# Performance work log

Measured on AMD Instinct MI355X. Metric: run time of the kernel, lower is better.

## Reference

```python
import jax, jax.numpy as jnp
import numpy as np

B, S, K_IN = 8, 2048, 512
D_MODEL, N_INPUT, N_PROCESS = 1024, 4096, 2048
K = 256


def setup_inputs() -> dict:
    key = jax.random.key(0)
    k1, k2, k3, k4 = jax.random.split(key, 4)
    return {
        "selected_activations": jax.random.normal(k1, (B, S, K_IN), dtype=jnp.float32),
        "selected_indices": jax.random.randint(k2, (B, K_IN), 0, N_INPUT, dtype=jnp.int64),
        "k": K,
        "combination_weights": jax.random.normal(k3, (N_PROCESS, N_INPUT), dtype=jnp.float32),
        "output_projections": jax.random.normal(k4, (N_PROCESS, D_MODEL), dtype=jnp.float32),
    }


def reference(selected_activations, selected_indices, k, combination_weights, output_projections):
    # Gather per-batch combination weights: [n_process, B, k_in] -> [B, n_process, k_in]
    sel_w = jnp.take(combination_weights, selected_indices, axis=1)  # [P, B, k_in]
    sel_w = jnp.transpose(sel_w, (1, 0, 2))                          # [B, P, k_in]
    # Batched matmul + exact GELU (torch F.gelu default is erf-based)
    process_act = jax.nn.gelu(
        jnp.einsum("bsk,bpk->bsp", selected_activations, sel_w), approximate=False
    )  # [B, S, P]
    # Top-k gating over mean activation across sequence
    process_scores = process_act.mean(axis=1)                        # [B, P]
    _, proc_idx = jax.lax.top_k(process_scores, k)                   # [B, k]
    # Gather selected process activations along last dim
    sel_proc_act = jnp.take_along_axis(process_act, proc_idx[:, None, :], axis=2)  # [B, S, k]
    # Gather output projections per batch: [B, k, d_model]
    sel_proj = output_projections[proc_idx]                          # [B, k, D]
    return jnp.einsum("bsk,bkd->bsd", sel_proc_act, sel_proj)        # [B, S, D]
```

## Files before the change

### kernel.cpp

```cpp
#include <hip/hip_runtime.h>
#include <hip/hip_bf16.h>
#include <math.h>

#define B_    8
#define S_    2048
#define KIN_  512
#define NIN_  4096
#define P_    2048
#define D_    1024
#define KSEL_ 256

typedef __attribute__((ext_vector_type(8))) short short8;
typedef __attribute__((ext_vector_type(4))) float f32x4;

__device__ __forceinline__ unsigned short f2bf(float f) {
    unsigned u = __float_as_uint(f);
    unsigned r = (u + 0x7fffu + ((u >> 16) & 1u)) >> 16;
    return (unsigned short)r;
}
__device__ __forceinline__ float bf2f(unsigned short h) {
    return __uint_as_float(((unsigned)h) << 16);
}
__device__ __forceinline__ float gelu_exact(float x) {
    return 0.5f * x * (1.0f + erff(x * 0.70710678118654752f));
}
__device__ __forceinline__ void gl2lds16(const void* g, void* l) {
    __builtin_amdgcn_global_load_lds(
        (const __attribute__((address_space(1))) unsigned int*)g,
        (__attribute__((address_space(3))) unsigned int*)l, 16, 0, 0);
}


__global__ __launch_bounds__(256) void prep_kernel(
        const float* __restrict__ A, const float* __restrict__ W,
        const int* __restrict__ idx,
        unsigned short* __restrict__ Ahi, unsigned short* __restrict__ AloF,
        unsigned short* __restrict__ Ghi, unsigned short* __restrict__ Glo) {
    __shared__ int ibs[KIN_];
    int id = blockIdx.x;
    int t  = threadIdx.x;
    if (id < 1024) {
        int b = id >> 7, rb = id & 127;
        int l = t & 63, wv = t >> 6;
        int lr = l & 15, quad = l >> 4;
        const float* src = A + ((size_t)(b * S_ + rb * 16 + lr)) * KIN_ + quad * 8;
        unsigned short* dh = Ahi + ((size_t)(b * S_ + rb * 16 + lr)) * KIN_ + quad * 8;
        unsigned short* dl = AloF + (size_t)b * 1048576 + (size_t)rb * 512 + (size_t)l * 8;
        for (int kb = wv; kb < 16; kb += 4) {
            float4 v0 = *(const float4*)(src + kb * 32);
            float4 v1 = *(const float4*)(src + kb * 32 + 4);
            float vv[8] = {v0.x, v0.y, v0.z, v0.w, v1.x, v1.y, v1.z, v1.w};
            short8 h8, l8;
#pragma unroll
            for (int jj = 0; jj < 8; jj++) {
                unsigned short h = f2bf(vv[jj]);
                h8[jj] = (short)h;
                l8[jj] = (short)f2bf(vv[jj] - bf2f(h));
            }
            *(short8*)(dh + kb * 32) = h8;
            *(short8*)(dl + (size_t)kb * 65536) = l8;
        }
    } else {
        int g = id - 1024;
        int b = g >> 9;
        ibs[t]       = idx[b * KIN_ + t];
        ibs[t + 256] = idx[b * KIN_ + t + 256];
        __syncthreads();
        int wv = t >> 6, tt = t & 63;
        int p  = (g * 4 + wv) & 2047;
        const float* wrow = W + (size_t)p * NIN_;
        size_t o = ((size_t)b * P_ + p) * KIN_;
        short8 h8, l8;
#pragma unroll
        for (int e = 0; e < 8; e++) {
            float v = wrow[ibs[tt * 8 + e]];
            unsigned short h = f2bf(v);
            h8[e] = (short)h;
            l8[e] = (short)f2bf(v - bf2f(h));
        }
        *(short8*)(Ghi + o + tt * 8) = h8;
        *(short8*)(Glo + o + tt * 8) = l8;
    }
}

template <bool STORE_C>
__global__ __launch_bounds__(256, 3) void gemm1_score(
        const unsigned short* __restrict__ Ahi, const unsigned short* __restrict__ AloF,
        const unsigned short* __restrict__ Ghi, const unsigned short* __restrict__ Glo,
        float* __restrict__ scores, unsigned short* __restrict__ C) {
    __shared__ __align__(16) unsigned short lds[24576];

    int d    = blockIdx.x;
    int xcd  = d & 7;
    int slot = d >> 3;
    int c    = (slot >> 4) * 8 + xcd;
    int j    = slot & 15;
    int b    = c >> 4;
    int rc   = c & 15;
    int p0   = ((rc & 3) * 4 + (j & 3)) * 128;
    int s0   = ((rc >> 2) * 4 + (j >> 2)) * 128;

    const int t  = threadIdx.x;
    const int w = t >> 6, l = t & 63;
    const int wm = w & 1, wn = w >> 1;
    const int lr = l & 15, quad = l >> 4;

    const int srow = t >> 2;
    const int koff = ((t & 3) ^ ((t >> 3) & 3)) * 8;
    const size_t baseA = ((size_t)(b * S_ + s0)) * KIN_;
    const size_t baseG = ((size_t)(b * P_ + p0)) * KIN_;
    const unsigned short* pA0 = Ahi + baseA + (size_t)srow * KIN_ + koff;
    const unsigned short* pA1 = pA0 + (size_t)64 * KIN_;
    const unsigned short* pG0 = Ghi + baseG + (size_t)srow * KIN_ + koff;
    const unsigned short* pG1 = pG0 + (size_t)64 * KIN_;
    const unsigned short* pH0 = Glo + baseG + (size_t)srow * KIN_ + koff;
    const unsigned short* pH1 = pH0 + (size_t)64 * KIN_;
    const unsigned short* alB = AloF + (size_t)b * 1048576
                              + (size_t)((s0 >> 4) + wm * 4) * 512 + (size_t)l * 8;
    char* lb = (char*)lds + w * 1024;

    int ra[4], rg[4];
#pragma unroll
    for (int i = 0; i < 4; i++) {
        int rowa = wm * 64 + i * 16 + lr;
        int rowg = wn * 64 + i * 16 + lr;
        ra[i] = rowa * 32 + (quad ^ ((rowa >> 1) & 3)) * 8;
        rg[i] = rowg * 32 + (quad ^ ((rowg >> 1) & 3)) * 8;
    }

    f32x4 acc[4][4];
#pragma unroll
    for (int i = 0; i < 4; i++)
#pragma unroll
        for (int jj = 0; jj < 4; jj++) acc[i][jj] = (f32x4){0.f, 0.f, 0.f, 0.f};

    auto issue = [&](int k0, int buf) {
        char* dst = lb + buf * 24576;
        gl2lds16(pA0 + k0, dst + 0);
        gl2lds16(pA1 + k0, dst + 4096);
        gl2lds16(pG0 + k0, dst + 8192);
        gl2lds16(pG1 + k0, dst + 12288);
        gl2lds16(pH0 + k0, dst + 16384);
        gl2lds16(pH1 + k0, dst + 20480);
    };

    issue(0, 0);
    for (int it = 0; it < KIN_ / 32; ++it) {
        short8 alc[4];
#pragma unroll
        for (int mt = 0; mt < 4; mt++)
            alc[mt] = *(const short8*)(alB + (size_t)it * 65536 + mt * 512);
        if (it + 1 < KIN_ / 32) {
            issue((it + 1) * 32, (it + 1) & 1);
            asm volatile("s_waitcnt vmcnt(10)\n\ts_barrier" ::: "memory");
        } else {
            asm volatile("s_waitcnt vmcnt(0)\n\ts_barrier" ::: "memory");
        }
        const unsigned short* Lb = lds + (it & 1) * 12288;

        short8 gh[4], gl8[4];
#pragma unroll
        for (int i = 0; i < 4; i++) {
            gh[i]  = *(const short8*)(Lb + 4096 + rg[i]);
            gl8[i] = *(const short8*)(Lb + 8192 + rg[i]);
        }
#pragma unroll
        for (int mt = 0; mt < 4; mt++) {
            short8 ah = *(const short8*)(Lb + ra[mt]);
#pragma unroll
            for (int nt = 0; nt < 4; nt++) {
                acc[mt][nt] = __builtin_amdgcn_mfma_f32_16x16x32_bf16(ah,      gh[nt],  acc[mt][nt], 0, 0, 0);
                acc[mt][nt] = __builtin_amdgcn_mfma_f32_16x16x32_bf16(ah,      gl8[nt], acc[mt][nt], 0, 0, 0);
                acc[mt][nt] = __builtin_amdgcn_mfma_f32_16x16x32_bf16(alc[mt], gh[nt],  acc[mt][nt], 0, 0, 0);
            }
        }
        asm volatile("s_barrier" ::: "memory");
    }

    float colsum[4] = {0.f, 0.f, 0.f, 0.f};
#pragma unroll
    for (int mt = 0; mt < 4; mt++)
#pragma unroll
        for (int nt = 0; nt < 4; nt++)
#pragma unroll
            for (int r = 0; r < 4; r++) {
                float g = gelu_exact(acc[mt][nt][r]);
                colsum[nt] += g;
                acc[mt][nt][r] = g;
            }
#pragma unroll
    for (int nt = 0; nt < 4; nt++) {
        colsum[nt] += __shfl_xor(colsum[nt], 16);
        colsum[nt] += __shfl_xor(colsum[nt], 32);
    }
    if (quad == 0) {
#pragma unroll
        for (int nt = 0; nt < 4; nt++)
            atomicAdd(&scores[b * P_ + p0 + wn * 64 + nt * 16 + lr], colsum[nt]);
    }

    if (STORE_C) {
#pragma unroll
        for (int mt = 0; mt < 4; mt++)
#pragma unroll
            for (int nt = 0; nt < 4; nt++)
#pragma unroll
                for (int r = 0; r < 4; r++) {
                    int row = wm * 64 + mt * 16 + quad * 4 + r;
                    int col = wn * 64 + nt * 16 + lr;
                    lds[row * 136 + col] = f2bf(acc[mt][nt][r]);
                }
        __syncthreads();
        for (int i = t; i < 2048; i += 256) {
            int row = i >> 4, ch = i & 15;
            uint4 v = *(const uint4*)(lds + row * 136 + ch * 8);
            *(uint4*)(C + ((size_t)(b * S_ + s0 + row)) * P_ + p0 + ch * 8) = v;
        }
    }
}

__global__ __launch_bounds__(1024) void topk_kernel(const float* __restrict__ scores,
                                                    int* __restrict__ pidx) {
    __shared__ float v[2048];
    __shared__ int   ix[2048];
    int b = blockIdx.x;
    int t = threadIdx.x;
    for (int i = t; i < 2048; i += 1024) { v[i] = scores[b * 2048 + i]; ix[i] = i; }
    __syncthreads();
    for (int k = 2; k <= 2048; k <<= 1) {
        for (int j = k >> 1; j > 0; j >>= 1) {
            for (int i = t; i < 2048; i += 1024) {
                int o = i ^ j;
                if (o > i) {
                    bool desc = ((i & k) == 0);
                    float va = v[i], vb = v[o];
                    int ia = ix[i], ib = ix[o];
                    bool b_first = (vb > va) || (vb == va && ib < ia);
                    if (desc == b_first) { v[i] = vb; v[o] = va; ix[i] = ib; ix[o] = ia; }
                }
            }
            __syncthreads();
        }
    }
    if (t < KSEL_) pidx[b * KSEL_ + t] = ix[t];
}

__global__ __launch_bounds__(256) void gathers_kernel(
        const unsigned short* __restrict__ C, const float* __restrict__ proj,
        const int* __restrict__ pidx,
        unsigned short* __restrict__ selact, unsigned short* __restrict__ PselT,
        int base) {
    __shared__ int pj[256];
    __shared__ unsigned short tile[64][65];
    int id = blockIdx.x + base, t = threadIdx.x;
    if (id < 2048) {
        int b = id >> 8;
        pj[t] = pidx[b * KSEL_ + t];
        __syncthreads();
        size_t r0 = (size_t)b * S_ + (id & 255) * 8;
#pragma unroll
        for (int r = 0; r < 8; ++r) {
            size_t row = r0 + r;
            selact[row * KSEL_ + t] = C[row * P_ + pj[t]];
        }
    } else {
        int g = id - 2048;
        int d0 = (g & 15) * 64, k0 = ((g >> 4) & 3) * 64, b = g >> 6;
        int tr = t >> 6;
        int tc = t & 63;
#pragma unroll
        for (int r = 0; r < 16; r++) {
            int kk = r * 4 + tr;
            int prow = pidx[b * KSEL_ + k0 + kk];
            tile[kk][tc] = f2bf(proj[(size_t)prow * D_ + d0 + tc]);
        }
        __syncthreads();
#pragma unroll
        for (int r = 0; r < 16; r++) {
            int dd = r * 4 + tr;
            PselT[((size_t)(b * D_ + d0 + dd)) * KSEL_ + k0 + tc] = tile[tc][dd];
        }
    }
}

__global__ __launch_bounds__(256) void gemm1b_selact(
        const unsigned short* __restrict__ Ahi, const unsigned short* __restrict__ AloF,
        const unsigned short* __restrict__ Ghi, const unsigned short* __restrict__ Glo,
        const int* __restrict__ pidx, unsigned short* __restrict__ selact) {
    __shared__ __align__(16) unsigned short lds[16384];

    const int t  = threadIdx.x;
    const int b  = blockIdx.z;
    const int s0 = blockIdx.y * 128;
    const int n0 = blockIdx.x * 128;
    const int w = t >> 6, l = t & 63;
    const int wm = w & 1, wn = w >> 1;
    const int lr = l & 15, quad = l >> 4;

    const int srow = t >> 2;
    const int koff = ((t & 3) ^ ((t >> 3) & 3)) * 8;
    const size_t baseA = ((size_t)(b * S_ + s0)) * KIN_;
    const size_t offA0 = baseA + (size_t)srow * KIN_ + koff;
    const size_t offA1 = offA0 + (size_t)64 * KIN_;
    const int prow0 = pidx[b * KSEL_ + n0 + srow];
    const int prow1 = pidx[b * KSEL_ + n0 + 64 + srow];
    const size_t offG0 = ((size_t)(b * P_ + prow0)) * KIN_ + koff;
    const size_t offG1 = ((size_t)(b * P_ + prow1)) * KIN_ + koff;
    const unsigned short* alB = AloF + (size_t)b * 1048576
                              + (size_t)((s0 >> 4) + wm * 4) * 512 + (size_t)l * 8;
    char* lb = (char*)lds + w * 1024;

    int ra[4], rg[4];
#pragma unroll
    for (int i = 0; i < 4; i++) {
        int rowa = wm * 64 + i * 16 + lr;
        int rowg = wn * 64 + i * 16 + lr;
        ra[i] = rowa * 32 + (quad ^ ((rowa >> 1) & 3)) * 8;
        rg[i] = rowg * 32 + (quad ^ ((rowg >> 1) & 3)) * 8;
    }

    f32x4 acc[4][4];
#pragma unroll
    for (int i = 0; i < 4; i++)
#pragma unroll
        for (int jj = 0; jj < 4; jj++) acc[i][jj] = (f32x4){0.f, 0.f, 0.f, 0.f};

    for (int k0 = 0; k0 < KIN_; k0 += 32) {
        int kb = k0 >> 5;
        gl2lds16(Ahi + offA0 + k0, lb + 0);
        gl2lds16(Ahi + offA1 + k0, lb + 4096);
        gl2lds16(Ghi + offG0 + k0, lb + 8192);
        gl2lds16(Ghi + offG1 + k0, lb + 12288);
        gl2lds16(Glo + offG0 + k0, lb + 16384);
        gl2lds16(Glo + offG1 + k0, lb + 20480);
        short8 alc[4];
#pragma unroll
        for (int i = 0; i < 4; i++)
            alc[i] = *(const short8*)(alB + (size_t)kb * 65536 + i * 512);
        __syncthreads();

        short8 gh[4], gl8[4];
#pragma unroll
        for (int i = 0; i < 4; i++) {
            gh[i]  = *(const short8*)(lds + 4096 + rg[i]);
            gl8[i] = *(const short8*)(lds + 8192 + rg[i]);
        }
#pragma unroll
        for (int mt = 0; mt < 4; mt++) {
            short8 ah = *(const short8*)(lds + ra[mt]);
#pragma unroll
            for (int nt = 0; nt < 4; nt++) {
                acc[mt][nt] = __builtin_amdgcn_mfma_f32_16x16x32_bf16(ah,      gh[nt],  acc[mt][nt], 0, 0, 0);
                acc[mt][nt] = __builtin_amdgcn_mfma_f32_16x16x32_bf16(ah,      gl8[nt], acc[mt][nt], 0, 0, 0);
                acc[mt][nt] = __builtin_amdgcn_mfma_f32_16x16x32_bf16(alc[mt], gh[nt],  acc[mt][nt], 0, 0, 0);
            }
        }
        __syncthreads();
    }

#pragma unroll
    for (int mt = 0; mt < 4; mt++)
#pragma unroll
        for (int nt = 0; nt < 4; nt++)
#pragma unroll
            for (int r = 0; r < 4; r++) {
                int row = wm * 64 + mt * 16 + quad * 4 + r;
                int col = wn * 64 + nt * 16 + lr;
                lds[row * 128 + col] = f2bf(gelu_exact(acc[mt][nt][r]));
            }
    __syncthreads();
    for (int i = t; i < 2048; i += 256) {
        int row = i >> 4, ch = i & 15;
        uint4 v = *(const uint4*)(lds + row * 128 + ch * 8);
        *(uint4*)(selact + ((size_t)(b * S_ + s0 + row)) * KSEL_ + n0 + ch * 8) = v;
    }
}

__global__ __launch_bounds__(256) void gemm2_mfma(
        const unsigned short* __restrict__ selact,
        const unsigned short* __restrict__ PselT,
        float* __restrict__ out) {
    __shared__ __align__(16) unsigned short lds[16384];

    const int t  = threadIdx.x;
    const int b  = blockIdx.z;
    const int s0 = blockIdx.y * 128;
    const int d0 = blockIdx.x * 128;
    const int w = t >> 6, l = t & 63;
    const int wm = w & 1, wn = w >> 1;
    const int lr = l & 15, quad = l >> 4;

    const int srow = t >> 2;
    const int koff = ((t & 3) ^ ((t >> 3) & 3)) * 8;
    const unsigned short* pA0 = selact + ((size_t)(b * S_ + s0 + srow)) * KSEL_ + koff;
    const unsigned short* pA1 = pA0 + (size_t)64 * KSEL_;
    const unsigned short* pB0 = PselT + ((size_t)(b * D_ + d0 + srow)) * KSEL_ + koff;
    const unsigned short* pB1 = pB0 + (size_t)64 * KSEL_;
    char* lb = (char*)lds + w * 1024;

    int ra[4], rg[4];
#pragma unroll
    for (int i = 0; i < 4; i++) {
        int rowa = wm * 64 + i * 16 + lr;
        int rowg = wn * 64 + i * 16 + lr;
        ra[i] = rowa * 32 + (quad ^ ((rowa >> 1) & 3)) * 8;
        rg[i] = rowg * 32 + (quad ^ ((rowg >> 1) & 3)) * 8;
    }

    f32x4 acc[4][4];
#pragma unroll
    for (int i = 0; i < 4; i++)
#pragma unroll
        for (int jj = 0; jj < 4; jj++) acc[i][jj] = (f32x4){0.f, 0.f, 0.f, 0.f};

    auto issue = [&](int k0, int buf) {
        char* dst = lb + buf * 16384;
        gl2lds16(pA0 + k0, dst + 0);
        gl2lds16(pA1 + k0, dst + 4096);
        gl2lds16(pB0 + k0, dst + 8192);
        gl2lds16(pB1 + k0, dst + 12288);
    };

    issue(0, 0);
    for (int it = 0; it < KSEL_ / 32; ++it) {
        if (it + 1 < KSEL_ / 32) {
            issue((it + 1) * 32, (it + 1) & 1);
            asm volatile("s_waitcnt vmcnt(4)\n\ts_barrier" ::: "memory");
        } else {
            asm volatile("s_waitcnt vmcnt(0)\n\ts_barrier" ::: "memory");
        }
        const unsigned short* Lb = lds + (it & 1) * 8192;

        short8 af[4], bf[4];
#pragma unroll
        for (int i = 0; i < 4; i++) {
            af[i] = *(const short8*)(Lb + ra[i]);
            bf[i] = *(const short8*)(Lb + 4096 + rg[i]);
        }
#pragma unroll
        for (int mt = 0; mt < 4; mt++)
#pragma unroll
            for (int nt = 0; nt < 4; nt++)
                acc[mt][nt] = __builtin_amdgcn_mfma_f32_16x16x32_bf16(af[mt], bf[nt], acc[mt][nt], 0, 0, 0);
        asm volatile("s_barrier" ::: "memory");
    }

#pragma unroll
    for (int mt = 0; mt < 4; mt++)
#pragma unroll
        for (int nt = 0; nt < 4; nt++)
#pragma unroll
            for (int r = 0; r < 4; r++)
                out[((size_t)(b * S_ + s0 + wm * 64 + mt * 16 + quad * 4 + r)) * D_
                    + d0 + wn * 64 + nt * 16 + lr] = acc[mt][nt][r];
}

extern "C" void kernel_launch(void* const* d_in, const int* in_sizes, int n_in,
                              void* d_out, int out_size, void* d_ws, size_t ws_size,
                              hipStream_t stream) {
    (void)in_sizes; (void)n_in; (void)out_size;
    const float* act  = (const float*)d_in[0];
    const int*   idx  = (const int*)d_in[1];
    const float* W    = (const float*)d_in[3];
    const float* proj = (const float*)d_in[4];
    float*       out  = (float*)d_out;

    char* ws = (char*)d_ws;
    unsigned short* Ahi    = (unsigned short*)(ws + 0);
    unsigned short* AloF   = (unsigned short*)(ws + 16777216);
    unsigned short* Ghi    = (unsigned short*)(ws + 33554432);
    unsigned short* Glo    = (unsigned short*)(ws + 50331648);
    float*          scores = (float*)(ws + 67108864);
    int*            pidx   = (int*)(ws + 67174400);
    unsigned short* selact = (unsigned short*)(ws + 67182592);
    unsigned short* PselT  = (unsigned short*)(ws + 75571200);
    unsigned short* Cbf    = (unsigned short*)(ws + 79765504);
    const bool big = ws_size >= 146874368ull;

    hipMemsetAsync(scores, 0, B_ * P_ * sizeof(float), stream);

    prep_kernel<<<dim3(1024 + (B_ * P_) / 4), 256, 0, stream>>>(act, W, idx, Ahi, AloF, Ghi, Glo);

    if (big) {
        gemm1_score<true><<<dim3(2048), 256, 0, stream>>>(Ahi, AloF, Ghi, Glo, scores, Cbf);
        topk_kernel<<<dim3(B_), 1024, 0, stream>>>(scores, pidx);
        gathers_kernel<<<dim3(2048 + 512), 256, 0, stream>>>(Cbf, proj, pidx, selact, PselT, 0);
    } else {
        gemm1_score<false><<<dim3(2048), 256, 0, stream>>>(Ahi, AloF, Ghi, Glo, scores, nullptr);
        topk_kernel<<<dim3(B_), 1024, 0, stream>>>(scores, pidx);
        gemm1b_selact<<<dim3(KSEL_ / 128, S_ / 128, B_), 256, 0, stream>>>(
            Ahi, AloF, Ghi, Glo, pidx, selact);
        gathers_kernel<<<dim3(512), 256, 0, stream>>>(Cbf, proj, pidx, selact, PselT, 2048);
    }
    gemm2_mfma<<<dim3(D_ / 128, S_ / 128, B_), 256, 0, stream>>>(selact, PselT, out);
}
```

Before: 356.6 us.

## Stage W rows in LDS once per process row and sort selected indices

Each prep block for the weight gather now loads one full combination-weight row into shared memory, along with all batch indices. It then produces the hi/lo bf16 gathered weights for all eight batches from LDS instead of doing random global reads per batch. The top-k kernel additionally sorts the selected process indices ascending to improve access locality in the downstream gathers. The cost is 32 KB of LDS per prep block, which can lower occupancy, plus extra bitonic passes in top-k.

```diff
diff --git a/kernel.cpp b/kernel.cpp
--- a/kernel.cpp
+++ b/kernel.cpp
@@ -36,7 +36,8 @@
         const int* __restrict__ idx,
         unsigned short* __restrict__ Ahi, unsigned short* __restrict__ AloF,
         unsigned short* __restrict__ Ghi, unsigned short* __restrict__ Glo) {
-    __shared__ int ibs[KIN_];
+    __shared__ float wrow_s[NIN_];
+    __shared__ int   ibs8[B_ * KIN_];
     int id = blockIdx.x;
     int t  = threadIdx.x;
     if (id < 1024) {
@@ -61,25 +62,33 @@
             *(short8*)(dl + (size_t)kb * 65536) = l8;
         }
     } else {
-        int g = id - 1024;
-        int b = g >> 9;
-        ibs[t]       = idx[b * KIN_ + t];
-        ibs[t + 256] = idx[b * KIN_ + t + 256];
+        int p = id - 1024;
+        const float* wrow = W + (size_t)p * NIN_;
+#pragma unroll
+        for (int i = 0; i < 4; i++)
+            *(float4*)(wrow_s + (t + i * 256) * 4) =
+                *(const float4*)(wrow + (t + i * 256) * 4);
+#pragma unroll
+        for (int i = 0; i < 16; i++)
+            ibs8[t + i * 256] = idx[t + i * 256];
         __syncthreads();
         int wv = t >> 6, tt = t & 63;
-        int p  = (g * 4 + wv) & 2047;
-        const float* wrow = W + (size_t)p * NIN_;
-        size_t o = ((size_t)b * P_ + p) * KIN_;
-        short8 h8, l8;
-#pragma unroll
-        for (int e = 0; e < 8; e++) {
-            float v = wrow[ibs[tt * 8 + e]];
-            unsigned short h = f2bf(v);
-            h8[e] = (short)h;
-            l8[e] = (short)f2bf(v - bf2f(h));
-        }
-        *(short8*)(Ghi + o + tt * 8) = h8;
-        *(short8*)(Glo + o + tt * 8) = l8;
+#pragma unroll
+        for (int bi = 0; bi < 2; ++bi) {
+            int b = wv * 2 + bi;
+            size_t o = ((size_t)b * P_ + p) * KIN_;
+            const int* ib = ibs8 + b * KIN_;
+            short8 h8, l8;
+#pragma unroll
+            for (int e = 0; e < 8; e++) {
+                float v = wrow_s[ib[tt * 8 + e]];
+                unsigned short h = f2bf(v);
+                h8[e] = (short)h;
+                l8[e] = (short)f2bf(v - bf2f(h));
+            }
+            *(short8*)(Ghi + o + tt * 8) = h8;
+            *(short8*)(Glo + o + tt * 8) = l8;
+        }
     }
 }
 
@@ -242,6 +251,19 @@
             __syncthreads();
         }
     }
+    for (int k = 2; k <= 256; k <<= 1) {
+        for (int j = k >> 1; j > 0; j >>= 1) {
+            if (t < 256) {
+                int i = t, o = i ^ j;
+                if (o > i) {
+                    bool asc = ((i & k) == 0);
+                    int a = ix[i], c2 = ix[o];
+                    if ((a > c2) == asc) { ix[i] = c2; ix[o] = a; }
+                }
+            }
+            __syncthreads();
+        }
+    }
     if (t < KSEL_) pidx[b * KSEL_ + t] = ix[t];
 }
 
@@ -479,7 +501,7 @@
 
     hipMemsetAsync(scores, 0, B_ * P_ * sizeof(float), stream);
 
-    prep_kernel<<<dim3(1024 + (B_ * P_) / 4), 256, 0, stream>>>(act, W, idx, Ahi, AloF, Ghi, Glo);
+    prep_kernel<<<dim3(1024 + P_), 256, 0, stream>>>(act, W, idx, Ahi, AloF, Ghi, Glo);
 
     if (big) {
         gemm1_score<true><<<dim3(2048), 256, 0, stream>>>(Ahi, AloF, Ghi, Glo, scores, Cbf);
```

New measurement: 355.6 us. No clear change (-0.3%).
